# Kernel optimization log

Measured on AMD Instinct MI355X. Metric: run time of the kernel, lower is better.

## Reference

```python
import jax, jax.numpy as jnp
import numpy as np

EPS = 1e-8

def squash(s, axis=-1):
    sq = jnp.sum(s * s, axis=axis, keepdims=True)
    return sq / (1.0 + sq) * s / (jnp.sqrt(sq) + EPS)

def setup_inputs() -> dict:
    key = jax.random.key(0)
    k1, k2 = jax.random.split(key)
    B, in_caps, in_dim = 256, 1152, 8
    num_caps, dim_caps = 10, 16
    x = jax.random.normal(k1, (B, in_caps, in_dim), dtype=jnp.float32)
    W = 0.01 * jax.random.normal(k2, (num_caps, in_caps, dim_caps, in_dim), dtype=jnp.float32)
    return {"x": x, "W": W}

def reference(x, W, num_routing=3):
    # u_hat: [B, num_caps, in_caps, dim_caps]
    u_hat = jnp.einsum('ncdi,bci->bncd', W, x)
    u_hat_det = jax.lax.stop_gradient(u_hat)
    B, N, C, D = u_hat.shape
    b = jnp.zeros((B, N, C, 1), dtype=u_hat.dtype)
    for _ in range(num_routing - 1):
        c = jax.nn.softmax(b, axis=1)                 # over num_caps
        s = jnp.sum(c * u_hat_det, axis=2)            # [B, N, D]
        v = squash(s)
        uv = jnp.einsum('bncd,bnd->bnc', u_hat_det, v)[..., None]
        b = b + uv
    c = jax.nn.softmax(b, axis=1)
    s = jnp.sum(c * u_hat, axis=2)
    v = squash(s)                                     # [B, N, D]
    return v
```

## Files before the change

kernel.cpp:

```cpp
#include <hip/hip_runtime.h>
#include <math.h>
#include <stdint.h>

#define B_N 256
#define C_N 1152
#define I_N 8
#define N_N 10
#define D_N 16

constexpr int C_PER    = 12;
constexpr int STAGE_C  = 4;
constexpr int N_STAGES = 3;
constexpr int C_CHUNKS = C_N / C_PER;
constexpr int B_TILE   = 16;
constexpr int BLOCK    = 256;

typedef short v8s __attribute__((ext_vector_type(8)));
typedef float v4f __attribute__((ext_vector_type(4)));

constexpr int POOL_BYTES = 16176 + 10496;

__device__ __forceinline__ uint32_t bf16_rne(float f) {
    uint32_t u = __float_as_uint(f);
    return (u + 0x7FFFu + ((u >> 16) & 1u)) >> 16;
}
__device__ __forceinline__ uint32_t pack2(float a, float b) {
    return bf16_rne(a) | (bf16_rne(b) << 16);
}
__device__ __forceinline__ float bf2f(short s) {
    return __uint_as_float(((uint32_t)(uint16_t)s) << 16);
}

template <bool FIRST>
__global__ __launch_bounds__(BLOCK, 6)
void route_pass(const float* __restrict__ x, const float* __restrict__ W,
                const float* __restrict__ vsum, float* __restrict__ p_s)
{
    __shared__ __align__(16) char pool[POOL_BYTES];
    short* Ws   = (short*)pool;
    short* xs   = (short*)(pool + 10240);
    float* cfl  = (float*)(pool + 13568);
    float* vss  = (float*)(pool + 16176);
    float* comb = (float*)(pool + 0);

    const int tid   = threadIdx.x;
    const int wv    = tid >> 6;
    const int lane  = tid & 63;
    const int b     = lane & 15;
    const int quad  = lane >> 4;
    const int chunk = blockIdx.x;
    const int gb0   = blockIdx.y * B_TILE;
    const int c0    = chunk * C_PER;

    {
        const float4* x4 = reinterpret_cast<const float4*>(x);
        #pragma unroll
        for (int it = 0; it < 2; ++it) {
            int e = (tid + BLOCK * it) * 4;
            if (e < 1536) {
                int b2 = e / 96, r = e - b2 * 96;
                float4 v = x4[(size_t)(gb0 + b2) * 2304 + chunk * 24 + (r >> 2)];
                *reinterpret_cast<uint2*>(xs + b2 * 104 + r) =
                    make_uint2(pack2(v.x, v.y), pack2(v.z, v.w));
            }
        }
    }
    if (!FIRST) {
        #pragma unroll
        for (int it = 0; it < 3; ++it) {
            int e = (tid + BLOCK * it) * 4;
            if (e < 2560) {
                int b2 = e / 160, r = e - b2 * 160;
                float4 v = *reinterpret_cast<const float4*>(
                    vsum + (size_t)(gb0 + b2) * 160 + r);
                *reinterpret_cast<float4*>(vss + b2 * 164 + r) = v;
            }
        }
    }

    const int ncnt = (wv < 2) ? 3 : 2;
    v4f sacc[3];
    sacc[0] = (v4f){0.f, 0.f, 0.f, 0.f};
    sacc[1] = (v4f){0.f, 0.f, 0.f, 0.f};
    sacc[2] = (v4f){0.f, 0.f, 0.f, 0.f};

    const float4* W4 = reinterpret_cast<const float4*>(W);

    for (int st = 0; st < N_STAGES; ++st) {
        __syncthreads();
        #pragma unroll
        for (int it = 0; it < 5; ++it) {
            int e = (tid + BLOCK * it) * 4;
            int n = e >> 9, rr = e & 511;
            int c = rr >> 7, k = rr & 127;
            float4 v = W4[(size_t)n * 36864 + (size_t)(c0 + st * STAGE_C + c) * 32 + (k >> 2)];
            *reinterpret_cast<uint2*>(Ws + c * 1280 + n * 128 + k) =
                make_uint2(pack2(v.x, v.y), pack2(v.z, v.w));
        }
        __syncthreads();

        if (!FIRST) {
            const int cl = wv;
            const v8s xb = *reinterpret_cast<const v8s*>(
                xs + b * 104 + (st * STAGE_C + cl) * 8);
            float Z = 0.f;
            #pragma unroll
            for (int n = 0; n < N_N; ++n) {
                v8s wa = {0, 0, 0, 0, 0, 0, 0, 0};
                if (quad == 0)
                    wa = *reinterpret_cast<const v8s*>(Ws + cl * 1280 + n * 128 + b * 8);
                v4f u = __builtin_amdgcn_mfma_f32_16x16x32_bf16(
                    wa, xb, (v4f){0.f, 0.f, 0.f, 0.f}, 0, 0, 0);
                const float4 vs4 = *reinterpret_cast<const float4*>(
                    vss + b * 164 + n * 16 + quad * 4);
                float l = u[0] * vs4.x + u[1] * vs4.y + u[2] * vs4.z + u[3] * vs4.w;
                l += __shfl_xor(l, 16);
                l += __shfl_xor(l, 32);
                const float e1 = __expf(l);
                Z += e1;
                if ((n & 3) == quad)
                    cfl[cl * 163 + n * 16 + b] = e1;
            }
            const float rz = __builtin_amdgcn_rcpf(Z);
            #pragma unroll
            for (int jj = 0; jj < 3; ++jj) {
                int n = 4 * jj + quad;
                if (n < N_N) cfl[cl * 163 + n * 16 + b] *= rz;
            }
            __syncthreads();
        }

        {
            const int cfull = st * STAGE_C + quad;
            const v8s xq = *reinterpret_cast<const v8s*>(xs + b * 104 + cfull * 8);
            float xf[8];
            #pragma unroll
            for (int j = 0; j < 8; ++j) xf[j] = bf2f(xq[j]);
            #pragma unroll
            for (int jj = 0; jj < 3; ++jj) {
                if (jj < ncnt) {
                    const int n = wv + 4 * jj;
                    const float cv = FIRST ? 0.1f : cfl[quad * 163 + n * 16 + b];
                    union { v8s s; uint32_t u[4]; } zu;
                    zu.u[0] = pack2(cv * xf[0], cv * xf[1]);
                    zu.u[1] = pack2(cv * xf[2], cv * xf[3]);
                    zu.u[2] = pack2(cv * xf[4], cv * xf[5]);
                    zu.u[3] = pack2(cv * xf[6], cv * xf[7]);
                    const v8s wa = *reinterpret_cast<const v8s*>(
                        Ws + quad * 1280 + n * 128 + b * 8);
                    sacc[jj] = __builtin_amdgcn_mfma_f32_16x16x32_bf16(
                        wa, zu.s, sacc[jj], 0, 0, 0);
                }
            }
        }
    }

    __syncthreads();
    #pragma unroll
    for (int jj = 0; jj < 3; ++jj) {
        if (jj < ncnt) {
            const int n = wv + 4 * jj;
            #pragma unroll
            for (int r = 0; r < 4; ++r)
                comb[b * 164 + n * 16 + quad * 4 + r] = sacc[jj][r];
        }
    }
    __syncthreads();
    #pragma unroll
    for (int it = 0; it < 3; ++it) {
        int f = tid + BLOCK * it;
        if (f < 640) {
            int e = f * 4;
            int bb = e / 160, rem = e - bb * 160;
            float4 v = *reinterpret_cast<const float4*>(comb + bb * 164 + rem);
            *reinterpret_cast<float4*>(
                &p_s[((size_t)chunk * B_N + gb0 + bb) * 160 + rem]) = v;
        }
    }
}

__global__ __launch_bounds__(BLOCK)
void reduce_squash(const float* __restrict__ p_s, float* __restrict__ vsum,
                   float* __restrict__ out, int phase)
{
    const int warp = threadIdx.x >> 6;
    const int lane = threadIdx.x & 63;
    const int g    = blockIdx.x * 4 + warp;
    const int q    = lane & 3;
    const int h    = lane >> 2;

    float4 s = make_float4(0.f, 0.f, 0.f, 0.f);
    #pragma unroll
    for (int m = 0; m < C_CHUNKS / 16; ++m) {
        const int cc = h + 16 * m;
        float4 v = *reinterpret_cast<const float4*>(
            &p_s[((size_t)cc * (B_N * N_N) + g) * D_N + q * 4]);
        s.x += v.x; s.y += v.y; s.z += v.z; s.w += v.w;
    }
    #pragma unroll
    for (int off = 4; off < 64; off <<= 1) {
        s.x += __shfl_xor(s.x, off);
        s.y += __shfl_xor(s.y, off);
        s.z += __shfl_xor(s.z, off);
        s.w += __shfl_xor(s.w, off);
    }
    float sq = s.x * s.x + s.y * s.y + s.z * s.z + s.w * s.w;
    sq += __shfl_xor(sq, 1);
    sq += __shfl_xor(sq, 2);

    const float scale = (sq / (1.f + sq)) / (sqrtf(sq) + 1e-8f);
    const float4 v = make_float4(scale * s.x, scale * s.y, scale * s.z, scale * s.w);

    if (h == 0) {
        if (phase == 0) {
            *reinterpret_cast<float4*>(&vsum[(size_t)g * D_N + q * 4]) = v;
        } else if (phase == 1) {
            float4 o = *reinterpret_cast<const float4*>(&vsum[(size_t)g * D_N + q * 4]);
            *reinterpret_cast<float4*>(&vsum[(size_t)g * D_N + q * 4]) =
                make_float4(o.x + v.x, o.y + v.y, o.z + v.z, o.w + v.w);
        } else {
            *reinterpret_cast<float4*>(&out[(size_t)g * D_N + q * 4]) = v;
        }
    }
}

extern "C" void kernel_launch(void* const* d_in, const int* in_sizes, int n_in,
                              void* d_out, int out_size, void* d_ws, size_t ws_size,
                              hipStream_t stream)
{
    const float* x = (const float*)d_in[0];
    const float* W = (const float*)d_in[1];
    float* out  = (float*)d_out;
    float* vsum = (float*)d_ws;
    float* p_s  = vsum + (size_t)B_N * N_N * D_N;

    dim3 grid(C_CHUNKS, B_N / B_TILE);
    dim3 blk(BLOCK);
    dim3 rgrid((B_N * N_N) / 4);

    route_pass<true><<<grid, blk, 0, stream>>>(x, W, nullptr, p_s);
    reduce_squash<<<rgrid, blk, 0, stream>>>(p_s, vsum, out, 0);
    route_pass<false><<<grid, blk, 0, stream>>>(x, W, vsum, p_s);
    reduce_squash<<<rgrid, blk, 0, stream>>>(p_s, vsum, out, 1);
    route_pass<false><<<grid, blk, 0, stream>>>(x, W, vsum, p_s);
    reduce_squash<<<rgrid, blk, 0, stream>>>(p_s, vsum, out, 2);
}
```

Baseline: 132.6 us.

## Pre-convert W and x to bf16 once and stream tiles via direct-to-LDS loads

Adds two prologue kernels that convert W and x to bf16 in layouts matching the shared-memory tiles. This removes repeated fp32 loads and per-pass bf16 conversion in each of the three routing passes. The route kernel now copies these tiles and the padded v-sum buffer into LDS with global_load_lds. The chunk size grows from 12 to 18 capsules, the softmax normalisation moves into a separate reciprocal step, and occupancy drops to 4 blocks. The cost is two extra launches and extra workspace traffic, and the larger LDS footprint lowers occupancy.

```diff
diff --git a/kernel.cpp b/kernel.cpp
--- a/kernel.cpp
+++ b/kernel.cpp
@@ -8,17 +8,26 @@
 #define N_N 10
 #define D_N 16
 
-constexpr int C_PER    = 12;
-constexpr int STAGE_C  = 4;
+constexpr int C_PER    = 18;
+constexpr int C_CHUNKS = C_N / C_PER;
+constexpr int STAGE_C  = 6;
 constexpr int N_STAGES = 3;
-constexpr int C_CHUNKS = C_N / C_PER;
-constexpr int B_TILE   = 16;
 constexpr int BLOCK    = 256;
 
 typedef short v8s __attribute__((ext_vector_type(8)));
 typedef float v4f __attribute__((ext_vector_type(4)));
 
-constexpr int POOL_BYTES = 16176 + 10496;
+constexpr int POOL_BYTES = 34760;
+
+constexpr size_t VSTG_FL = 16 * 16 * 164;
+constexpr size_t PS_FL   = (size_t)C_CHUNKS * B_N * 160;
+constexpr size_t WB_SH   = (size_t)C_N * 1280;
+constexpr size_t XT_SH   = (size_t)1024 * 2304;
+
+#define GLD16(g, l)                                                         \
+    __builtin_amdgcn_global_load_lds(                                       \
+        (const uint32_t __attribute__((address_space(1)))*)(g),             \
+        (uint32_t __attribute__((address_space(3)))*)(l), 16, 0, 0)
 
 __device__ __forceinline__ uint32_t bf16_rne(float f) {
     uint32_t u = __float_as_uint(f);
@@ -31,17 +40,56 @@
     return __uint_as_float(((uint32_t)(uint16_t)s) << 16);
 }
 
+__global__ __launch_bounds__(BLOCK)
+void conv_w(const float* __restrict__ W, short* __restrict__ Wb)
+{
+    const int c0 = blockIdx.x * 8;
+    const int cc = threadIdx.x >> 5;
+    const int k4 = threadIdx.x & 31;
+    const float4* W4 = (const float4*)W;
+    uint2* dst = (uint2*)Wb;
+    for (int n = 0; n < N_N; ++n) {
+        float4 v = W4[(size_t)n * 36864 + (size_t)(c0 + cc) * 32 + k4];
+        dst[(((size_t)(c0 + cc) * 1280 + n * 128) >> 2) + k4] =
+            make_uint2(pack2(v.x, v.y), pack2(v.z, v.w));
+    }
+}
+
+__global__ __launch_bounds__(BLOCK)
+void conv_x(const float* __restrict__ x, short* __restrict__ xt)
+{
+    const int tile  = blockIdx.x;
+    const int chunk = tile >> 4;
+    const int btile = tile & 15;
+    const int c0    = chunk * C_PER;
+    const int gb0   = btile * 16;
+    const float4* x4 = (const float4*)x;
+    uint2* dst = (uint2*)(xt + (size_t)tile * 2304);
+    #pragma unroll
+    for (int it = 0; it < 3; ++it) {
+        int f = threadIdx.x + BLOCK * it;
+        if (f < 576) {
+            int b = f / 36, r = f - b * 36;
+            float4 v = x4[(size_t)(gb0 + b) * 2304 + c0 * 2 + r];
+            int cp = r >> 1, i0 = (r & 1) * 4;
+            dst[((cp * 128 + b * 8 + i0) >> 2)] =
+                make_uint2(pack2(v.x, v.y), pack2(v.z, v.w));
+        }
+    }
+}
+
 template <bool FIRST>
-__global__ __launch_bounds__(BLOCK, 6)
-void route_pass(const float* __restrict__ x, const float* __restrict__ W,
-                const float* __restrict__ vsum, float* __restrict__ p_s)
+__global__ __launch_bounds__(BLOCK, 4)
+void route_pass(const short* __restrict__ Wb, const short* __restrict__ xt,
+                const float* __restrict__ vstG, float* __restrict__ p_s)
 {
     __shared__ __align__(16) char pool[POOL_BYTES];
     short* Ws   = (short*)pool;
-    short* xs   = (short*)(pool + 10240);
-    float* cfl  = (float*)(pool + 13568);
-    float* vss  = (float*)(pool + 16176);
-    float* comb = (float*)(pool + 0);
+    short* xs   = (short*)(pool + 15360);
+    float* vst  = (float*)(pool + 19968);
+    float* cfl  = (float*)(pool + 30464);
+    float* rz   = (float*)(pool + 34376);
+    float* comb = (float*)pool;
 
     const int tid   = threadIdx.x;
     const int wv    = tid >> 6;
@@ -49,32 +97,24 @@
     const int b     = lane & 15;
     const int quad  = lane >> 4;
     const int chunk = blockIdx.x;
-    const int gb0   = blockIdx.y * B_TILE;
+    const int btile = blockIdx.y;
+    const int gb0   = btile * 16;
     const int c0    = chunk * C_PER;
 
     {
-        const float4* x4 = reinterpret_cast<const float4*>(x);
+        const char* src = (const char*)(xt + (size_t)(chunk * 16 + btile) * 2304);
         #pragma unroll
         for (int it = 0; it < 2; ++it) {
-            int e = (tid + BLOCK * it) * 4;
-            if (e < 1536) {
-                int b2 = e / 96, r = e - b2 * 96;
-                float4 v = x4[(size_t)(gb0 + b2) * 2304 + chunk * 24 + (r >> 2)];
-                *reinterpret_cast<uint2*>(xs + b2 * 104 + r) =
-                    make_uint2(pack2(v.x, v.y), pack2(v.z, v.w));
-            }
+            int f = tid + BLOCK * it;
+            if (f < 288) GLD16(src + f * 16, (char*)xs + f * 16);
         }
     }
     if (!FIRST) {
+        const char* src = (const char*)(vstG + (size_t)btile * 2624);
         #pragma unroll
         for (int it = 0; it < 3; ++it) {
-            int e = (tid + BLOCK * it) * 4;
-            if (e < 2560) {
-                int b2 = e / 160, r = e - b2 * 160;
-                float4 v = *reinterpret_cast<const float4*>(
-                    vsum + (size_t)(gb0 + b2) * 160 + r);
-                *reinterpret_cast<float4*>(vss + b2 * 164 + r) = v;
-            }
+            int f = tid + BLOCK * it;
+            if (f < 656) GLD16(src + f * 16, (char*)vst + f * 16);
         }
     }
 
@@ -84,55 +124,54 @@
     sacc[1] = (v4f){0.f, 0.f, 0.f, 0.f};
     sacc[2] = (v4f){0.f, 0.f, 0.f, 0.f};
 
-    const float4* W4 = reinterpret_cast<const float4*>(W);
-
     for (int st = 0; st < N_STAGES; ++st) {
         __syncthreads();
-        #pragma unroll
-        for (int it = 0; it < 5; ++it) {
-            int e = (tid + BLOCK * it) * 4;
-            int n = e >> 9, rr = e & 511;
-            int c = rr >> 7, k = rr & 127;
-            float4 v = W4[(size_t)n * 36864 + (size_t)(c0 + st * STAGE_C + c) * 32 + (k >> 2)];
-            *reinterpret_cast<uint2*>(Ws + c * 1280 + n * 128 + k) =
-                make_uint2(pack2(v.x, v.y), pack2(v.z, v.w));
+        {
+            const char* src = (const char*)(Wb + (size_t)(c0 + st * STAGE_C) * 1280);
+            #pragma unroll
+            for (int it = 0; it < 4; ++it) {
+                int f = tid + BLOCK * it;
+                if (f < 960) GLD16(src + f * 16, (char*)Ws + f * 16);
+            }
         }
         __syncthreads();
 
         if (!FIRST) {
-            const int cl = wv;
-            const v8s xb = *reinterpret_cast<const v8s*>(
-                xs + b * 104 + (st * STAGE_C + cl) * 8);
-            float Z = 0.f;
-            #pragma unroll
-            for (int n = 0; n < N_N; ++n) {
+            #pragma unroll
+            for (int k = 0; k < 15; ++k) {
+                const int idx = wv + 4 * k;
+                const int c   = idx / 10;
+                const int n   = idx - c * 10;
                 v8s wa = {0, 0, 0, 0, 0, 0, 0, 0};
                 if (quad == 0)
-                    wa = *reinterpret_cast<const v8s*>(Ws + cl * 1280 + n * 128 + b * 8);
+                    wa = *(const v8s*)(Ws + c * 1280 + n * 128 + b * 8);
+                const v8s xb = *(const v8s*)(xs + (st * STAGE_C + c) * 128 + b * 8);
                 v4f u = __builtin_amdgcn_mfma_f32_16x16x32_bf16(
                     wa, xb, (v4f){0.f, 0.f, 0.f, 0.f}, 0, 0, 0);
-                const float4 vs4 = *reinterpret_cast<const float4*>(
-                    vss + b * 164 + n * 16 + quad * 4);
-                float l = u[0] * vs4.x + u[1] * vs4.y + u[2] * vs4.z + u[3] * vs4.w;
+                const float4 v4 = *(const float4*)(vst + b * 164 + n * 16 + quad * 4);
+                float l = u[0] * v4.x + u[1] * v4.y + u[2] * v4.z + u[3] * v4.w;
                 l += __shfl_xor(l, 16);
                 l += __shfl_xor(l, 32);
                 const float e1 = __expf(l);
-                Z += e1;
-                if ((n & 3) == quad)
-                    cfl[cl * 163 + n * 16 + b] = e1;
-            }
-            const float rz = __builtin_amdgcn_rcpf(Z);
-            #pragma unroll
-            for (int jj = 0; jj < 3; ++jj) {
-                int n = 4 * jj + quad;
-                if (n < N_N) cfl[cl * 163 + n * 16 + b] *= rz;
+                if (quad == 0) cfl[c * 163 + n * 16 + b] = e1;
             }
             __syncthreads();
-        }
-
-        {
-            const int cfull = st * STAGE_C + quad;
-            const v8s xq = *reinterpret_cast<const v8s*>(xs + b * 104 + cfull * 8);
+            if (tid < 96) {
+                const int c = tid >> 4, bb = tid & 15;
+                float Z = 0.f;
+                #pragma unroll
+                for (int n = 0; n < N_N; ++n) Z += cfl[c * 163 + n * 16 + bb];
+                rz[c * 16 + bb] = __builtin_amdgcn_rcpf(Z);
+            }
+            __syncthreads();
+        }
+
+        #pragma unroll
+        for (int Q = 0; Q < 2; ++Q) {
+            const int  clq   = Q * 4 + quad;
+            const bool valid = (clq < STAGE_C);
+            const int  clql  = valid ? clq : 0;
+            const v8s xq = *(const v8s*)(xs + (st * STAGE_C + clql) * 128 + b * 8);
             float xf[8];
             #pragma unroll
             for (int j = 0; j < 8; ++j) xf[j] = bf2f(xq[j]);
@@ -140,14 +179,16 @@
             for (int jj = 0; jj < 3; ++jj) {
                 if (jj < ncnt) {
                     const int n = wv + 4 * jj;
-                    const float cv = FIRST ? 0.1f : cfl[quad * 163 + n * 16 + b];
+                    const float cv = FIRST ? 0.1f
+                        : cfl[clql * 163 + n * 16 + b] * rz[clql * 16 + b];
                     union { v8s s; uint32_t u[4]; } zu;
                     zu.u[0] = pack2(cv * xf[0], cv * xf[1]);
                     zu.u[1] = pack2(cv * xf[2], cv * xf[3]);
                     zu.u[2] = pack2(cv * xf[4], cv * xf[5]);
                     zu.u[3] = pack2(cv * xf[6], cv * xf[7]);
-                    const v8s wa = *reinterpret_cast<const v8s*>(
-                        Ws + quad * 1280 + n * 128 + b * 8);
+                    v8s wa = {0, 0, 0, 0, 0, 0, 0, 0};
+                    if (valid)
+                        wa = *(const v8s*)(Ws + clql * 1280 + n * 128 + b * 8);
                     sacc[jj] = __builtin_amdgcn_mfma_f32_16x16x32_bf16(
                         wa, zu.s, sacc[jj], 0, 0, 0);
                 }
@@ -172,15 +213,14 @@
         if (f < 640) {
             int e = f * 4;
             int bb = e / 160, rem = e - bb * 160;
-            float4 v = *reinterpret_cast<const float4*>(comb + bb * 164 + rem);
-            *reinterpret_cast<float4*>(
-                &p_s[((size_t)chunk * B_N + gb0 + bb) * 160 + rem]) = v;
+            float4 v = *(const float4*)(comb + bb * 164 + rem);
+            *(float4*)(&p_s[((size_t)chunk * B_N + gb0 + bb) * 160 + rem]) = v;
         }
     }
 }
 
 __global__ __launch_bounds__(BLOCK)
-void reduce_squash(const float* __restrict__ p_s, float* __restrict__ vsum,
+void reduce_squash(const float* __restrict__ p_s, float* __restrict__ vstG,
                    float* __restrict__ out, int phase)
 {
     const int warp = threadIdx.x >> 6;
@@ -193,8 +233,7 @@
     #pragma unroll
     for (int m = 0; m < C_CHUNKS / 16; ++m) {
         const int cc = h + 16 * m;
-        float4 v = *reinterpret_cast<const float4*>(
-            &p_s[((size_t)cc * (B_N * N_N) + g) * D_N + q * 4]);
+        float4 v = *(const float4*)(&p_s[((size_t)cc * (B_N * N_N) + g) * D_N + q * 4]);
         s.x += v.x; s.y += v.y; s.z += v.z; s.w += v.w;
     }
     #pragma unroll
@@ -212,14 +251,17 @@
     const float4 v = make_float4(scale * s.x, scale * s.y, scale * s.z, scale * s.w);
 
     if (h == 0) {
-        if (phase == 0) {
-            *reinterpret_cast<float4*>(&vsum[(size_t)g * D_N + q * 4]) = v;
-        } else if (phase == 1) {
-            float4 o = *reinterpret_cast<const float4*>(&vsum[(size_t)g * D_N + q * 4]);
-            *reinterpret_cast<float4*>(&vsum[(size_t)g * D_N + q * 4]) =
-                make_float4(o.x + v.x, o.y + v.y, o.z + v.z, o.w + v.w);
+        if (phase == 2) {
+            *(float4*)(&out[(size_t)g * D_N + q * 4]) = v;
         } else {
-            *reinterpret_cast<float4*>(&out[(size_t)g * D_N + q * 4]) = v;
+            const int bb = g / 10, n = g - bb * 10;
+            float* vp = vstG + (size_t)(bb >> 4) * 2624 + (bb & 15) * 164 + n * 16 + q * 4;
+            if (phase == 0) {
+                *(float4*)vp = v;
+            } else {
+                float4 o = *(const float4*)vp;
+                *(float4*)vp = make_float4(o.x + v.x, o.y + v.y, o.z + v.z, o.w + v.w);
+            }
         }
     }
 }
@@ -231,17 +273,22 @@
     const float* x = (const float*)d_in[0];
     const float* W = (const float*)d_in[1];
     float* out  = (float*)d_out;
-    float* vsum = (float*)d_ws;
-    float* p_s  = vsum + (size_t)B_N * N_N * D_N;
-
-    dim3 grid(C_CHUNKS, B_N / B_TILE);
-    dim3 blk(BLOCK);
+
+    float* vstG = (float*)d_ws;
+    float* p_s  = vstG + VSTG_FL;
+    short* Wb   = (short*)(p_s + PS_FL);
+    short* xt   = Wb + WB_SH;
+
+    conv_w<<<dim3(C_N / 8), BLOCK, 0, stream>>>(W, Wb);
+    conv_x<<<dim3(1024), BLOCK, 0, stream>>>(x, xt);
+
+    dim3 grid(C_CHUNKS, 16);
     dim3 rgrid((B_N * N_N) / 4);
 
-    route_pass<true><<<grid, blk, 0, stream>>>(x, W, nullptr, p_s);
-    reduce_squash<<<rgrid, blk, 0, stream>>>(p_s, vsum, out, 0);
-    route_pass<false><<<grid, blk, 0, stream>>>(x, W, vsum, p_s);
-    reduce_squash<<<rgrid, blk, 0, stream>>>(p_s, vsum, out, 1);
-    route_pass<false><<<grid, blk, 0, stream>>>(x, W, vsum, p_s);
-    reduce_squash<<<rgrid, blk, 0, stream>>>(p_s, vsum, out, 2);
-}
+    route_pass<true><<<grid, BLOCK, 0, stream>>>(Wb, xt, vstG, p_s);
+    reduce_squash<<<rgrid, BLOCK, 0, stream>>>(p_s, vstG, out, 0);
+    route_pass<false><<<grid, BLOCK, 0, stream>>>(Wb, xt, vstG, p_s);
+    reduce_squash<<<rgrid, BLOCK, 0, stream>>>(p_s, vstG, out, 1);
+    route_pass<false><<<grid, BLOCK, 0, stream>>>(Wb, xt, vstG, p_s);
+    reduce_squash<<<rgrid, BLOCK, 0, stream>>>(p_s, vstG, out, 2);
+}
```

After: 130.4 us. No clear change (-1.7%).
